# Kernel optimization log

Measured on AMD Instinct MI355X. Metric: run time of the kernel, lower is better.

Reference implementation:

```python
import jax, jax.numpy as jnp
import numpy as np

D, H, BS, K_TOP = 2560, 32, 32, 16
HD = D // H  # 80
B, S = 2, 1024
SCALE = HD ** -0.5


def setup_inputs() -> dict:
    key = jax.random.key(0)
    ks = jax.random.split(key, 10)
    sc = 0.02

    def lin(k, i, o):
        return (jax.random.normal(k, (i, o), jnp.float32) * sc,
                jnp.zeros((o,), jnp.float32))

    Wq, bq = lin(ks[0], D, D)
    Wk, bk = lin(ks[1], D, D)
    Wv, bv = lin(ks[2], D, D)
    Wo, bo = lin(ks[3], D, D)
    comp_W1, comp_b1 = lin(ks[4], BS * HD, 4 * HD)
    comp_W2, comp_b2 = lin(ks[5], 4 * HD, HD)
    comp_pos = jax.random.normal(ks[6], (BS, HD), jnp.float32) * sc
    gate_W1, gate_b1 = lin(ks[7], D, D // 2)
    gate_W2, gate_b2 = lin(ks[8], D // 2, 3)
    hidden_states = jax.random.normal(ks[9], (B, S, D), jnp.float32)
    return dict(hidden_states=hidden_states, Wq=Wq, bq=bq, Wk=Wk, bk=bk,
                Wv=Wv, bv=bv, Wo=Wo, bo=bo, comp_pos=comp_pos,
                comp_W1=comp_W1, comp_b1=comp_b1, comp_W2=comp_W2,
                comp_b2=comp_b2, gate_W1=gate_W1, gate_b1=gate_b1,
                gate_W2=gate_W2, gate_b2=gate_b2)


def reference(hidden_states, Wq, bq, Wk, bk, Wv, bv, Wo, bo, comp_pos,
              comp_W1, comp_b1, comp_W2, comp_b2, gate_W1, gate_b1,
              gate_W2, gate_b2):
    b, s, dm = hidden_states.shape
    blocks = s // BS

    def heads(y):  # [b,s,D] -> [b,H,s,hd]
        return y.reshape(b, s, H, HD).transpose(0, 2, 1, 3)

    q = heads(hidden_states @ Wq + bq)
    k = heads(hidden_states @ Wk + bk)
    v = heads(hidden_states @ Wv + bv)

    # --- compression branch: per-head block compression MLP (shared K/V) ---
    def compress(t):  # [b,H,s,hd] -> [b,H,blocks,hd]
        tb = t.reshape(b, H, blocks, BS, HD) + comp_pos  # pos emb per block slot
        tb = tb.reshape(b, H, blocks, BS * HD)
        h1 = jax.nn.gelu(tb @ comp_W1 + comp_b1, approximate=False)
        return h1 @ comp_W2 + comp_b2

    kc = compress(k)
    vc = compress(v)
    attn_c = jax.nn.softmax(jnp.einsum('bhsd,bhnd->bhsn', q, kc) * SCALE, axis=-1)
    out_c = jnp.einsum('bhsn,bhnd->bhsd', attn_c, vc)

    # --- dense scores, shared by selection scoring and window branch ---
    scores = jnp.einsum('bhqd,bhkd->bhqk', q, k) * SCALE  # [b,H,s,s]

    # --- selection branch: per-query top-k blocks by block-mean score ---
    block_scores = scores.reshape(b, H, s, blocks, BS).mean(-1)  # [b,H,s,blocks]
    _, top_idx = jax.lax.top_k(block_scores, K_TOP)  # [b,H,s,K]
    sel = (jnp.arange(blocks)[None, None, None, None, :] == top_idx[..., None]).any(-2)
    key_mask = jnp.repeat(sel, BS, axis=-1)  # [b,H,s,s]
    sel_scores = jnp.where(key_mask, scores, -jnp.inf)
    out_s = jnp.einsum('bhqk,bhkd->bhqd', jax.nn.softmax(sel_scores, axis=-1), v)

    # --- window branch: source's window mask is all-ones -> full attention ---
    out_w = jnp.einsum('bhqk,bhkd->bhqd', jax.nn.softmax(scores, axis=-1), v)

    # --- learned gates ---
    gh = jax.nn.gelu(hidden_states @ gate_W1 + gate_b1, approximate=False)
    gates = jax.nn.sigmoid(gh @ gate_W2 + gate_b2)  # [b,s,3]
    g = gates.transpose(2, 0, 1)[:, :, None, :, None]  # [3,b,1,s,1]
    combined = g[0] * out_c + g[1] * out_s + g[2] * out_w  # [b,H,s,hd]
    combined = combined.transpose(0, 2, 1, 3).reshape(b, s, dm)
    return combined @ Wo + bo
```

## Files before the change

### kernel.cpp

```cpp
#include <hip/hip_runtime.h>
#include <hip/hip_bf16.h>
#include <math.h>

typedef unsigned short u16;
typedef short v8s __attribute__((ext_vector_type(8)));
typedef float v4f __attribute__((ext_vector_type(4)));

#define SCALE_F 0.11180339887498949f

__device__ __forceinline__ float bf2f(u16 x) {
    unsigned int u = ((unsigned int)x) << 16;
    return __builtin_bit_cast(float, u);
}
__device__ __forceinline__ u16 f2bf(float f) {
    unsigned int u = __builtin_bit_cast(unsigned int, f);
    unsigned int r = (u + 0x7FFFu + ((u >> 16) & 1u)) >> 16;
    return (u16)r;
}
__device__ __forceinline__ float scrub(float v) {
    return (fabsf(v) < 1e30f) ? v : 0.f;
}
__device__ __forceinline__ v8s zero8() {
    union { v8s v; short s[8]; } t;
#pragma unroll
    for (int i = 0; i < 8; i++) t.s[i] = 0;
    return t.v;
}

__global__ void convX_kernel(const float* __restrict__ X, u16* __restrict__ Xb, int n)
{
    int i = (blockIdx.x * 256 + threadIdx.x) * 4;
    if (i >= n) return;
    float4 v = *(const float4*)(X + i);
    u16 o[4] = { f2bf(v.x), f2bf(v.y), f2bf(v.z), f2bf(v.w) };
    *(uint2*)(Xb + i) = *(uint2*)o;
}

__global__ __launch_bounds__(256) void convT_kernel(
    const float* __restrict__ W, u16* __restrict__ WT, int K, int N)
{
    __shared__ float t[32][33];
    int n0 = blockIdx.x * 32, k0 = blockIdx.y * 32;
    int tx = threadIdx.x & 31, ty = threadIdx.x >> 5;
    for (int i = ty; i < 32; i += 8) {
        int k = k0 + i, n = n0 + tx;
        t[i][tx] = (k < K && n < N) ? W[(size_t)k * N + n] : 0.f;
    }
    __syncthreads();
    for (int i = ty; i < 32; i += 8) {
        int n = n0 + i, k = k0 + tx;
        if (n < N && k < K) WT[(size_t)n * K + k] = f2bf(t[tx][i]);
    }
}

__global__ void xmean_kernel(const float* __restrict__ X, float* __restrict__ Xm)
{
    int c = blockIdx.x * 256 + threadIdx.x;
    if (c >= 2560) return;
    int g = blockIdx.y;
    const float* base = X + (size_t)g * 32 * 2560 + c;
    float s = 0.f;
#pragma unroll 4
    for (int j = 0; j < 32; j++) s += base[(size_t)j * 2560];
    Xm[(size_t)g * 2560 + c] = s * (1.f / 32.f);
}

__global__ __launch_bounds__(256) void gemmS_kernel(
    const float* __restrict__ A, const float* __restrict__ B,
    const float* __restrict__ bias, int M, int N, int K, float* __restrict__ outf)
{
    __shared__ __align__(16) u16 Ah[64][32], Al[64][32];
    __shared__ __align__(16) u16 Bh[64][32], Bl[64][32];
    const int tid = threadIdx.x;
    const int bm = blockIdx.x * 64, bn = blockIdx.y * 64;
    const int w = tid >> 6, lane = tid & 63;
    const int quad = lane >> 4, l = lane & 15;
    v4f acc[4];
#pragma unroll
    for (int nt = 0; nt < 4; nt++)
#pragma unroll
        for (int r = 0; r < 4; r++) acc[nt][r] = 0.f;
    const int ar = tid >> 2, ak = (tid & 3) * 8;
    const int kr = tid >> 3, nc = (tid & 7) * 8;
    for (int k0 = 0; k0 < K; k0 += 32) {
        float4 a0 = *(const float4*)(A + (size_t)(bm + ar) * K + (k0 + ak));
        float4 a1 = *(const float4*)(A + (size_t)(bm + ar) * K + (k0 + ak) + 4);
        float4 b0 = *(const float4*)(B + (size_t)(k0 + kr) * N + (bn + nc));
        float4 b1 = *(const float4*)(B + (size_t)(k0 + kr) * N + (bn + nc) + 4);
        float av[8] = {a0.x,a0.y,a0.z,a0.w,a1.x,a1.y,a1.z,a1.w};
        float bv[8] = {b0.x,b0.y,b0.z,b0.w,b1.x,b1.y,b1.z,b1.w};
        __syncthreads();
#pragma unroll
        for (int j = 0; j < 8; j++) {
            u16 h = f2bf(av[j]);
            Ah[ar][ak + j] = h; Al[ar][ak + j] = f2bf(av[j] - bf2f(h));
            u16 g = f2bf(bv[j]);
            Bh[nc + j][kr] = g; Bl[nc + j][kr] = f2bf(bv[j] - bf2f(g));
        }
        __syncthreads();
        v8s ah = *(const v8s*)(&Ah[w * 16 + l][quad * 8]);
        v8s al = *(const v8s*)(&Al[w * 16 + l][quad * 8]);
#pragma unroll
        for (int nt = 0; nt < 4; nt++) {
            v8s bh = *(const v8s*)(&Bh[nt * 16 + l][quad * 8]);
            v8s bl = *(const v8s*)(&Bl[nt * 16 + l][quad * 8]);
            acc[nt] = __builtin_amdgcn_mfma_f32_16x16x32_bf16(ah, bh, acc[nt], 0, 0, 0);
            acc[nt] = __builtin_amdgcn_mfma_f32_16x16x32_bf16(ah, bl, acc[nt], 0, 0, 0);
            acc[nt] = __builtin_amdgcn_mfma_f32_16x16x32_bf16(al, bh, acc[nt], 0, 0, 0);
        }
    }
#pragma unroll
    for (int nt = 0; nt < 4; nt++) {
        int col = bn + nt * 16 + l;
        float bvs = bias[col];
#pragma unroll
        for (int r = 0; r < 4; r++) {
            int row = bm + w * 16 + quad * 4 + r;
            outf[(size_t)row * N + col] = scrub(acc[nt][r] + bvs);
        }
    }
}

__global__ __launch_bounds__(256) void m1_kernel(
    const float* __restrict__ Wq, const float* __restrict__ km,
    u16* __restrict__ M1hT, u16* __restrict__ M1lT)
{
    __shared__ float Ws[64][81];
    __shared__ float Ks[32][80];
    int k0 = blockIdx.x * 64, h = blockIdx.y, b = blockIdx.z;
    int tid = threadIdx.x;
    for (int i = tid; i < 64 * 80; i += 256) {
        int kk = i / 80, dd = i - kk * 80;
        Ws[kk][dd] = Wq[(size_t)(k0 + kk) * 2560 + h * 80 + dd];
    }
    for (int i = tid; i < 32 * 80; i += 256) {
        int bl = i / 80, dd = i - bl * 80;
        Ks[bl][dd] = km[(size_t)((b << 5) + bl) * 2560 + h * 80 + dd];
    }
    __syncthreads();
    int kk = tid & 63, bq4 = tid >> 6;
    for (int bt = 0; bt < 8; bt++) {
        int blk = bt * 4 + bq4;
        float s = 0.f;
#pragma unroll 8
        for (int d = 0; d < 80; d++) s += Ws[kk][d] * Ks[blk][d];
        u16 hi = f2bf(s);
        size_t o = (size_t)(b * 1024 + h * 32 + blk) * 2560 + k0 + kk;
        M1hT[o] = hi;
        M1lT[o] = f2bf(s - bf2f(hi));
    }
}

__global__ void bias3_kernel(const float* __restrict__ bq, const float* __restrict__ km,
                             float* __restrict__ bias3)
{
    int i = blockIdx.x * 256 + threadIdx.x;
    if (i >= 2048) return;
    int b = i >> 10, hb = i & 1023, h = hb >> 5, blk = hb & 31;
    float s = 0.f;
    for (int d = 0; d < 80; d++) s += bq[h * 80 + d] * km[(size_t)((b << 5) + blk) * 2560 + h * 80 + d];
    bias3[i] = s;
}

__global__ __launch_bounds__(256) void gemmS2_kernel(
    const float* __restrict__ A, const u16* __restrict__ BhT, const u16* __restrict__ BlT,
    const float* __restrict__ bias, int M, int N, int K, float* __restrict__ outf)
{
    __shared__ __align__(16) u16 Ah[64][32], Al[64][32];
    __shared__ __align__(16) u16 Bh[64][32], Bl[64][32];
    const int tid = threadIdx.x;
    const int bm = blockIdx.x * 64, bn = blockIdx.y * 64;
    const int w = tid >> 6, lane = tid & 63;
    const int quad = lane >> 4, l = lane & 15;
    v4f acc[4];
#pragma unroll
    for (int nt = 0; nt < 4; nt++)
#pragma unroll
        for (int r = 0; r < 4; r++) acc[nt][r] = 0.f;
    const int ar = tid >> 2, ak = (tid & 3) * 8;
    for (int k0 = 0; k0 < K; k0 += 32) {
        float4 a0 = *(const float4*)(A + (size_t)(bm + ar) * K + (k0 + ak));
        float4 a1 = *(const float4*)(A + (size_t)(bm + ar) * K + (k0 + ak) + 4);
        float av[8] = {a0.x,a0.y,a0.z,a0.w,a1.x,a1.y,a1.z,a1.w};
        uint4 bh8 = *(const uint4*)(BhT + (size_t)(bn + ar) * K + (k0 + ak));
        uint4 bl8 = *(const uint4*)(BlT + (size_t)(bn + ar) * K + (k0 + ak));
        __syncthreads();
#pragma unroll
        for (int j = 0; j < 8; j++) {
            u16 h = f2bf(av[j]);
            Ah[ar][ak + j] = h; Al[ar][ak + j] = f2bf(av[j] - bf2f(h));
        }
        *(uint4*)(&Bh[ar][ak]) = bh8;
        *(uint4*)(&Bl[ar][ak]) = bl8;
        __syncthreads();
        v8s ah = *(const v8s*)(&Ah[w * 16 + l][quad * 8]);
        v8s al = *(const v8s*)(&Al[w * 16 + l][quad * 8]);
#pragma unroll
        for (int nt = 0; nt < 4; nt++) {
            v8s bh = *(const v8s*)(&Bh[nt * 16 + l][quad * 8]);
            v8s bl = *(const v8s*)(&Bl[nt * 16 + l][quad * 8]);
            acc[nt] = __builtin_amdgcn_mfma_f32_16x16x32_bf16(ah, bh, acc[nt], 0, 0, 0);
            acc[nt] = __builtin_amdgcn_mfma_f32_16x16x32_bf16(ah, bl, acc[nt], 0, 0, 0);
            acc[nt] = __builtin_amdgcn_mfma_f32_16x16x32_bf16(al, bh, acc[nt], 0, 0, 0);
        }
    }
#pragma unroll
    for (int nt = 0; nt < 4; nt++) {
        int col = bn + nt * 16 + l;
        float bvs = bias[col];
#pragma unroll
        for (int r = 0; r < 4; r++) {
            int row = bm + w * 16 + quad * 4 + r;
            outf[(size_t)row * N + col] = scrub(acc[nt][r] + bvs);
        }
    }
}

__global__ __launch_bounds__(256) void gemmB_kernel(
    const u16* __restrict__ A, const u16* __restrict__ Al2, const u16* __restrict__ BT,
    const float* __restrict__ bias, int M, int N, int K, int act, int ldc,
    u16* __restrict__ outb, float* __restrict__ outf, u16* __restrict__ outT)
{
    __shared__ __align__(16) u16 As[64][32];
    __shared__ __align__(16) u16 As2[64][32];
    __shared__ __align__(16) u16 Bs[64][32];
    const int tid = threadIdx.x;
    const int bm = blockIdx.x * 64, bn = blockIdx.y * 64;
    const int w = tid >> 6, lane = tid & 63;
    const int quad = lane >> 4, l = lane & 15;
    v4f acc[4];
#pragma unroll
    for (int nt = 0; nt < 4; nt++)
#pragma unroll
        for (int r = 0; r < 4; r++) acc[nt][r] = 0.f;
    const int ar = tid >> 2, ak = (tid & 3) * 8;
    for (int k0 = 0; k0 < K; k0 += 32) {
        uint4 av = *(const uint4*)(A + (size_t)(bm + ar) * K + (k0 + ak));
        uint4 av2 = make_uint4(0,0,0,0);
        if (Al2) av2 = *(const uint4*)(Al2 + (size_t)(bm + ar) * K + (k0 + ak));
        uint4 bv = make_uint4(0,0,0,0);
        if (bn + ar < N) bv = *(const uint4*)(BT + (size_t)(bn + ar) * K + (k0 + ak));
        __syncthreads();
        *(uint4*)(&As[ar][ak]) = av;
        if (Al2) *(uint4*)(&As2[ar][ak]) = av2;
        *(uint4*)(&Bs[ar][ak]) = bv;
        __syncthreads();
        v8s af = *(const v8s*)(&As[w * 16 + l][quad * 8]);
#pragma unroll
        for (int nt = 0; nt < 4; nt++) {
            v8s bf = *(const v8s*)(&Bs[nt * 16 + l][quad * 8]);
            acc[nt] = __builtin_amdgcn_mfma_f32_16x16x32_bf16(af, bf, acc[nt], 0, 0, 0);
        }
        if (Al2) {
            v8s af2 = *(const v8s*)(&As2[w * 16 + l][quad * 8]);
#pragma unroll
            for (int nt = 0; nt < 4; nt++) {
                v8s bf = *(const v8s*)(&Bs[nt * 16 + l][quad * 8]);
                acc[nt] = __builtin_amdgcn_mfma_f32_16x16x32_bf16(af2, bf, acc[nt], 0, 0, 0);
            }
        }
    }
#pragma unroll
    for (int nt = 0; nt < 4; nt++) {
        int col = bn + nt * 16 + l;
        if (col < N) {
            float bvs = bias[col];
#pragma unroll
            for (int r = 0; r < 4; r++) {
                int row = bm + w * 16 + quad * 4 + r;
                float c = acc[nt][r] + bvs;
                if (act == 1) c = 0.5f * c * (1.0f + erff(c * 0.70710678118654752f));
                c = scrub(c);
                if (outf) outf[(size_t)row * ldc + col] = c;
                if (outb) outb[(size_t)row * ldc + col] = f2bf(c);
                if (outT) {
                    int bb = row >> 10, s = row & 1023;
                    int hh = col / 80, dd = col - hh * 80;
                    outT[((size_t)((bb << 5) + hh) * 96 + dd) * 1024 + s] = f2bf(c);
                }
            }
        }
    }
}

__global__ void padv_kernel(u16* __restrict__ vt)
{
    int i = blockIdx.x * 256 + threadIdx.x;
    if (i >= 64 * 16 * 1024) return;
    int s = i & 1023, rr = (i >> 10) & 15, bh = i >> 14;
    vt[((size_t)bh * 96 + 80 + rr) * 1024 + s] = (rr == 0) ? (u16)0x3F80 : (u16)0;
}

__global__ void gatherF_kernel(const u16* __restrict__ src, const float* __restrict__ pos,
                               u16* __restrict__ F)
{
    int row = blockIdx.y;
    int col = blockIdx.x * 256 + threadIdx.x;
    if (col >= 2560) return;
    int b = row >> 10, h = (row >> 5) & 31, blk = row & 31;
    int j = col / 80, d = col - j * 80;
    float v = bf2f(src[(size_t)(b * 1024 + blk * 32 + j) * 2560 + h * 80 + d]) + pos[col];
    F[(size_t)row * 2560 + col] = f2bf(v);
}
__global__ void gatherFT_kernel(const u16* __restrict__ vt, const float* __restrict__ pos,
                                u16* __restrict__ F)
{
    int row = blockIdx.y;
    int col = blockIdx.x * 256 + threadIdx.x;
    if (col >= 2560) return;
    int b = row >> 10, h = (row >> 5) & 31, blk = row & 31;
    int j = col / 80, d = col - j * 80;
    float v = bf2f(vt[((size_t)((b << 5) + h) * 96 + d) * 1024 + blk * 32 + j]) + pos[col];
    F[(size_t)row * 2560 + col] = f2bf(v);
}

__global__ __launch_bounds__(256) void gates_kernel(
    const u16* __restrict__ gh, const float* __restrict__ W2,
    const float* __restrict__ b2, float* __restrict__ gates)
{
    int w = threadIdx.x >> 6, lane = threadIdx.x & 63;
    int token = blockIdx.x * 4 + w;
    float s0 = 0.f, s1 = 0.f, s2 = 0.f;
    for (int i = lane; i < 1280; i += 64) {
        float g = bf2f(gh[(size_t)token * 1280 + i]);
        s0 += g * W2[i * 3 + 0];
        s1 += g * W2[i * 3 + 1];
        s2 += g * W2[i * 3 + 2];
    }
#pragma unroll
    for (int m = 1; m < 64; m <<= 1) {
        s0 += __shfl_xor(s0, m);
        s1 += __shfl_xor(s1, m);
        s2 += __shfl_xor(s2, m);
    }
    if (lane == 0) {
        gates[token * 3 + 0] = scrub(1.f / (1.f + expf(-(s0 + b2[0]))));
        gates[token * 3 + 1] = scrub(1.f / (1.f + expf(-(s1 + b2[1]))));
        gates[token * 3 + 2] = scrub(1.f / (1.f + expf(-(s2 + b2[2]))));
    }
}

__global__ __launch_bounds__(64) void attn_kernel(
    const u16* __restrict__ qb, const u16* __restrict__ kbf,
    const u16* __restrict__ vt, const u16* __restrict__ kc,
    const u16* __restrict__ vc, const float* __restrict__ BSf,
    const float* __restrict__ gates, u16* __restrict__ comb, u16* __restrict__ combl)
{
    const int lane = threadIdx.x, quad = lane >> 4, l = lane & 15;
    const int qt = blockIdx.x, bh = blockIdx.y, b = bh >> 5, h = bh & 31;
    const float NEG = -1e30f;

    __shared__ float bs[16][33];
    __shared__ unsigned int selmask[16];
    __shared__ __align__(16) u16 Pw[16][40];

    {
        const float* bsrow = BSf + ((size_t)b * 1024 + qt * 16 + l) * 1024 + h * 32 + quad * 8;
#pragma unroll
        for (int i = 0; i < 8; i++) bs[l][quad * 8 + i] = bsrow[i] * SCALE_F;
    }
    __syncthreads();
    if (lane < 16) {
        unsigned int mask = 0u;
        for (int it = 0; it < 16; it++) {
            float best = NEG; int bi = -1;
            for (int n = 0; n < 32; n++) {
                if (((mask >> n) & 1u) == 0u && bs[lane][n] > best) { best = bs[lane][n]; bi = n; }
            }
            if (bi < 0) { for (int n = 0; n < 32; n++) if (((mask >> n) & 1u) == 0u) { bi = n; break; } }
            mask |= (1u << bi);
        }
        selmask[lane] = mask;
    }
    __syncthreads();
    const unsigned int selm_l = selmask[l];
    unsigned int selm[4];
#pragma unroll
    for (int r = 0; r < 4; r++) selm[r] = selmask[quad * 4 + r];
    (void)selm;

    v8s qfrag[3];
    {
        const u16* qrow = qb + (size_t)(b * 1024 + qt * 16 + l) * 2560 + h * 80;
#pragma unroll
        for (int c = 0; c < 3; c++) {
            if (c == 2 && quad >= 2) { qfrag[c] = zero8(); }
            else qfrag[c] = *(const v8s*)(qrow + c * 32 + quad * 8);
        }
    }

    v4f oc[5];
#pragma unroll
    for (int t = 0; t < 5; t++)
#pragma unroll
        for (int r = 0; r < 4; r++) oc[t][r] = 0.f;
    float l_c[4];
    {
        v4f s0, s1;
#pragma unroll
        for (int r = 0; r < 4; r++) { s0[r] = 0.f; s1[r] = 0.f; }
#pragma unroll
        for (int c = 0; c < 3; c++) {
            v8s b0, b1;
            if (c == 2 && quad >= 2) { b0 = zero8(); b1 = zero8(); }
            else {
                b0 = *(const v8s*)(kc + (size_t)(bh * 32 + l) * 80 + c * 32 + quad * 8);
                b1 = *(const v8s*)(kc + (size_t)(bh * 32 + 16 + l) * 80 + c * 32 + quad * 8);
            }
            s0 = __builtin_amdgcn_mfma_f32_16x16x32_bf16(qfrag[c], b0, s0, 0, 0, 0);
            s1 = __builtin_amdgcn_mfma_f32_16x16x32_bf16(qfrag[c], b1, s1, 0, 0, 0);
        }
#pragma unroll
        for (int r = 0; r < 4; r++) {
            float x0 = s0[r] * SCALE_F, x1 = s1[r] * SCALE_F;
            float mx = fmaxf(x0, x1);
#pragma unroll
            for (int m = 1; m < 16; m <<= 1) mx = fmaxf(mx, __shfl_xor(mx, m));
            float p0 = expf(x0 - mx), p1 = expf(x1 - mx);
            float sm = p0 + p1;
#pragma unroll
            for (int m = 1; m < 16; m <<= 1) sm += __shfl_xor(sm, m);
            l_c[r] = sm;
            Pw[quad * 4 + r][l]      = f2bf(p0);
            Pw[quad * 4 + r][l + 16] = f2bf(p1);
        }
        __syncthreads();
        v8s pa = *(const v8s*)(&Pw[l][quad * 8]);
#pragma unroll
        for (int t = 0; t < 5; t++) {
            union { v8s v; short s[8]; } vf;
#pragma unroll
            for (int j = 0; j < 8; j++)
                vf.s[j] = (short)vc[(size_t)(bh * 32 + quad * 8 + j) * 80 + t * 16 + l];
            oc[t] = __builtin_amdgcn_mfma_f32_16x16x32_bf16(pa, vf.v, oc[t], 0, 0, 0);
        }
        __syncthreads();
    }

    v4f aw[6], as_[6];
    float m_w[4];
#pragma unroll
    for (int r = 0; r < 4; r++) m_w[r] = NEG;
#pragma unroll
    for (int t = 0; t < 6; t++)
#pragma unroll
        for (int r = 0; r < 4; r++) { aw[t][r] = 0.f; as_[t][r] = 0.f; }

    const u16* vtp = vt + (size_t)bh * 96 * 1024;

    for (int kb = 0; kb < 32; kb++) {
        v4f s0, s1;
#pragma unroll
        for (int r = 0; r < 4; r++) { s0[r] = 0.f; s1[r] = 0.f; }
#pragma unroll
        for (int c = 0; c < 3; c++) {
            v8s k0f, k1f;
            if (c == 2 && quad >= 2) { k0f = zero8(); k1f = zero8(); }
            else {
                size_t base = (size_t)(b * 1024 + kb * 32) * 2560 + h * 80 + c * 32 + quad * 8;
                k0f = *(const v8s*)(kbf + base + (size_t)l * 2560);
                k1f = *(const v8s*)(kbf + base + (size_t)(16 + l) * 2560);
            }
            s0 = __builtin_amdgcn_mfma_f32_16x16x32_bf16(qfrag[c], k0f, s0, 0, 0, 0);
            s1 = __builtin_amdgcn_mfma_f32_16x16x32_bf16(qfrag[c], k1f, s1, 0, 0, 0);
        }
        float alw[4];
#pragma unroll
        for (int r = 0; r < 4; r++) {
            float x0 = s0[r] * SCALE_F, x1 = s1[r] * SCALE_F;
            float mb = fmaxf(x0, x1);
#pragma unroll
            for (int m = 1; m < 16; m <<= 1) mb = fmaxf(mb, __shfl_xor(mb, m));
            float mn = fmaxf(m_w[r], mb);
            alw[r] = expf(m_w[r] - mn);
            m_w[r] = mn;
            Pw[quad * 4 + r][l]      = f2bf(expf(x0 - mn));
            Pw[quad * 4 + r][l + 16] = f2bf(expf(x1 - mn));
        }
        __syncthreads();
        v8s pwa = *(const v8s*)(&Pw[l][quad * 8]);
        v8s psa = ((selm_l >> kb) & 1u) ? pwa : zero8();
#pragma unroll
        for (int t = 0; t < 6; t++) {
            v8s vfr = *(const v8s*)(vtp + ((size_t)(t * 16 + l)) * 1024 + kb * 32 + quad * 8);
#pragma unroll
            for (int r = 0; r < 4; r++) { aw[t][r] *= alw[r]; as_[t][r] *= alw[r]; }
            aw[t]  = __builtin_amdgcn_mfma_f32_16x16x32_bf16(pwa, vfr, aw[t], 0, 0, 0);
            as_[t] = __builtin_amdgcn_mfma_f32_16x16x32_bf16(psa, vfr, as_[t], 0, 0, 0);
        }
        __syncthreads();
    }

    float l_w[4], l_s[4];
#pragma unroll
    for (int r = 0; r < 4; r++) {
        l_w[r] = __shfl(aw[5][r], quad * 16);
        l_s[r] = __shfl(as_[5][r], quad * 16);
    }

#pragma unroll
    for (int r = 0; r < 4; r++) {
        int token = b * 1024 + qt * 16 + quad * 4 + r;
        float g0 = gates[token * 3 + 0], g1 = gates[token * 3 + 1], g2 = gates[token * 3 + 2];
        float inv_w = 1.f / fmaxf(l_w[r], 1e-30f);
        float inv_s = 1.f / fmaxf(l_s[r], 1e-30f);
        float inv_c = 1.f / fmaxf(l_c[r], 1e-30f);
#pragma unroll
        for (int t = 0; t < 5; t++) {
            float val = g0 * (oc[t][r] * inv_c) + g1 * (as_[t][r] * inv_s) + g2 * (aw[t][r] * inv_w);
            val = scrub(val);
            u16 hi = f2bf(val);
            size_t o = (size_t)token * 2560 + h * 80 + t * 16 + l;
            comb[o] = hi;
            combl[o] = f2bf(val - bf2f(hi));
        }
    }
}

extern "C" void kernel_launch(void* const* d_in, const int* in_sizes, int n_in,
                              void* d_out, int out_size, void* d_ws, size_t ws_size,
                              hipStream_t stream)
{
    (void)in_sizes; (void)n_in; (void)out_size; (void)ws_size;

    const float* X   = (const float*)d_in[0];
    const float* Wq  = (const float*)d_in[1];
    const float* bq  = (const float*)d_in[2];
    const float* Wk  = (const float*)d_in[3];
    const float* bk  = (const float*)d_in[4];
    const float* Wv  = (const float*)d_in[5];
    const float* bv  = (const float*)d_in[6];
    const float* Wo  = (const float*)d_in[7];
    const float* bo  = (const float*)d_in[8];
    const float* pos = (const float*)d_in[9];
    const float* cW1 = (const float*)d_in[10];
    const float* cb1 = (const float*)d_in[11];
    const float* cW2 = (const float*)d_in[12];
    const float* cb2 = (const float*)d_in[13];
    const float* gW1 = (const float*)d_in[14];
    const float* gb1 = (const float*)d_in[15];
    const float* gW2 = (const float*)d_in[16];
    const float* gb2 = (const float*)d_in[17];

    char* ws = (char*)d_ws;
    size_t off = 0;
    auto alloc = [&](size_t bytes) -> void* {
        void* p = ws + off;
        off += (bytes + 255) & ~(size_t)255;
        return p;
    };
    u16*   Xb     = (u16*)  alloc(2048ull * 2560 * 2);
    u16*   WqT    = (u16*)  alloc(2560ull * 2560 * 2);
    u16*   WkT    = (u16*)  alloc(2560ull * 2560 * 2);
    u16*   WvT    = (u16*)  alloc(2560ull * 2560 * 2);
    u16*   WoT    = (u16*)  alloc(2560ull * 2560 * 2);
    u16*   gW1T   = (u16*)  alloc(1280ull * 2560 * 2);
    u16*   cW1T   = (u16*)  alloc(320ull * 2560 * 2);
    u16*   cW2T   = (u16*)  alloc(96ull * 320 * 2);
    float* Xm     = (float*)alloc(64ull * 2560 * 4);
    float* kmeanS = (float*)alloc(64ull * 2560 * 4);
    u16*   M1hT   = (u16*)  alloc(2048ull * 2560 * 2);
    u16*   M1lT   = (u16*)  alloc(2048ull * 2560 * 2);
    float* bias3  = (float*)alloc(2048ull * 4);
    u16*   qbuf   = (u16*)  alloc(2048ull * 2560 * 2);
    u16*   kbf    = (u16*)  alloc(2048ull * 2560 * 2);
    u16*   vtb    = (u16*)  alloc(64ull * 96 * 1024 * 2);
    u16*   combl  = (u16*)  alloc(2048ull * 2560 * 2);
    char*  R1     = (char*) alloc(12ull * 1024 * 1024);
    u16*   gh     = (u16*)R1;
    u16*   Fb     = (u16*)R1;
    u16*   H1     = (u16*)(R1 + 10ull * 1024 * 1024);
    u16*   combb  = (u16*)R1;
    u16*   KC     = (u16*)  alloc(2048ull * 80 * 2);
    u16*   VC     = (u16*)  alloc(2048ull * 80 * 2);
    float* gatesf = (float*)alloc(2048ull * 3 * 4);
    float* BSf    = (float*)d_out;

    dim3 blk(256);
    convX_kernel<<<2048 * 2560 / 4 / 256, blk, 0, stream>>>(X, Xb, 2048 * 2560);
    convT_kernel<<<dim3(80, 80), blk, 0, stream>>>(Wq, WqT, 2560, 2560);
    convT_kernel<<<dim3(80, 80), blk, 0, stream>>>(Wk, WkT, 2560, 2560);
    convT_kernel<<<dim3(80, 80), blk, 0, stream>>>(Wv, WvT, 2560, 2560);
    convT_kernel<<<dim3(80, 80), blk, 0, stream>>>(Wo, WoT, 2560, 2560);
    convT_kernel<<<dim3(40, 80), blk, 0, stream>>>(gW1, gW1T, 2560, 1280);
    convT_kernel<<<dim3(10, 80), blk, 0, stream>>>(cW1, cW1T, 2560, 320);
    convT_kernel<<<dim3(3, 10), blk, 0, stream>>>(cW2, cW2T, 320, 80);
    xmean_kernel<<<dim3(10, 64), blk, 0, stream>>>(X, Xm);
    gemmS_kernel<<<dim3(1, 40), blk, 0, stream>>>(Xm, Wk, bk, 64, 2560, 2560, kmeanS);
    m1_kernel<<<dim3(40, 32, 2), blk, 0, stream>>>(Wq, kmeanS, M1hT, M1lT);
    bias3_kernel<<<8, blk, 0, stream>>>(bq, kmeanS, bias3);
    for (int b = 0; b < 2; b++) {
        gemmS2_kernel<<<dim3(16, 16), blk, 0, stream>>>(
            X + (size_t)b * 1024 * 2560, M1hT + (size_t)b * 1024 * 2560,
            M1lT + (size_t)b * 1024 * 2560, bias3 + b * 1024,
            1024, 1024, 2560, BSf + (size_t)b * 1024 * 1024);
    }
    gemmB_kernel<<<dim3(32, 40), blk, 0, stream>>>(Xb, nullptr, WqT, bq, 2048, 2560, 2560, 0, 2560, qbuf, nullptr, nullptr);
    gemmB_kernel<<<dim3(32, 40), blk, 0, stream>>>(Xb, nullptr, WkT, bk, 2048, 2560, 2560, 0, 2560, kbf, nullptr, nullptr);
    gemmB_kernel<<<dim3(32, 40), blk, 0, stream>>>(Xb, nullptr, WvT, bv, 2048, 2560, 2560, 0, 2560, nullptr, nullptr, vtb);
    padv_kernel<<<4096, blk, 0, stream>>>(vtb);
    gemmB_kernel<<<dim3(32, 20), blk, 0, stream>>>(Xb, nullptr, gW1T, gb1, 2048, 1280, 2560, 1, 1280, gh, nullptr, nullptr);
    gates_kernel<<<512, blk, 0, stream>>>(gh, gW2, gb2, gatesf);
    gatherF_kernel<<<dim3(10, 2048), blk, 0, stream>>>(kbf, pos, Fb);
    gemmB_kernel<<<dim3(32, 5), blk, 0, stream>>>(Fb, nullptr, cW1T, cb1, 2048, 320, 2560, 1, 320, H1, nullptr, nullptr);
    gemmB_kernel<<<dim3(32, 2), blk, 0, stream>>>(H1, nullptr, cW2T, cb2, 2048, 80, 320, 0, 80, KC, nullptr, nullptr);
    gatherFT_kernel<<<dim3(10, 2048), blk, 0, stream>>>(vtb, pos, Fb);
    gemmB_kernel<<<dim3(32, 5), blk, 0, stream>>>(Fb, nullptr, cW1T, cb1, 2048, 320, 2560, 1, 320, H1, nullptr, nullptr);
    gemmB_kernel<<<dim3(32, 2), blk, 0, stream>>>(H1, nullptr, cW2T, cb2, 2048, 80, 320, 0, 80, VC, nullptr, nullptr);
    attn_kernel<<<dim3(64, 64), 64, 0, stream>>>(qbuf, kbf, vtb, KC, VC, BSf, gatesf, combb, combl);
    gemmB_kernel<<<dim3(32, 40), blk, 0, stream>>>(combb, combl, WoT, bo, 2048, 2560, 2560, 0, 2560, nullptr, (float*)d_out, nullptr);
}
```

Before: 1.250 ms.

## Use direct global-to-LDS loads in GEMM and streamline attention softmax

```diff
diff --git a/kernel.cpp b/kernel.cpp
--- a/kernel.cpp
+++ b/kernel.cpp
@@ -7,6 +7,7 @@
 typedef float v4f __attribute__((ext_vector_type(4)));
 
 #define SCALE_F 0.11180339887498949f
+#define SCALE_L2 0.16129821534f
 
 __device__ __forceinline__ float bf2f(u16 x) {
     unsigned int u = ((unsigned int)x) << 16;
@@ -25,6 +26,11 @@
 #pragma unroll
     for (int i = 0; i < 8; i++) t.s[i] = 0;
     return t.v;
+}
+__device__ __forceinline__ void glds16(const void* g, void* s) {
+    __builtin_amdgcn_global_load_lds(
+        (const __attribute__((address_space(1))) unsigned int*)g,
+        (__attribute__((address_space(3))) unsigned int*)s, 16, 0, 0);
 }
 
 __global__ void convX_kernel(const float* __restrict__ X, u16* __restrict__ Xb, int n)
@@ -234,16 +240,18 @@
 #pragma unroll
         for (int r = 0; r < 4; r++) acc[nt][r] = 0.f;
     const int ar = tid >> 2, ak = (tid & 3) * 8;
+    const int brow = (bn + ar < N) ? (bn + ar) : (N - 1);
+    const u16* Ap = A + (size_t)(bm + ar) * K + ak;
+    const u16* Bp = BT + (size_t)brow * K + ak;
+    const u16* A2p = Al2 ? (Al2 + (size_t)(bm + ar) * K + ak) : nullptr;
+    char* AsW  = ((char*)As)  + w * 1024;
+    char* As2W = ((char*)As2) + w * 1024;
+    char* BsW  = ((char*)Bs)  + w * 1024;
     for (int k0 = 0; k0 < K; k0 += 32) {
-        uint4 av = *(const uint4*)(A + (size_t)(bm + ar) * K + (k0 + ak));
-        uint4 av2 = make_uint4(0,0,0,0);
-        if (Al2) av2 = *(const uint4*)(Al2 + (size_t)(bm + ar) * K + (k0 + ak));
-        uint4 bv = make_uint4(0,0,0,0);
-        if (bn + ar < N) bv = *(const uint4*)(BT + (size_t)(bn + ar) * K + (k0 + ak));
-        __syncthreads();
-        *(uint4*)(&As[ar][ak]) = av;
-        if (Al2) *(uint4*)(&As2[ar][ak]) = av2;
-        *(uint4*)(&Bs[ar][ak]) = bv;
+        __syncthreads();
+        glds16(Ap + k0, AsW);
+        glds16(Bp + k0, BsW);
+        if (Al2) glds16(A2p + k0, As2W);
         __syncthreads();
         v8s af = *(const v8s*)(&As[w * 16 + l][quad * 8]);
 #pragma unroll
@@ -283,14 +291,6 @@
     }
 }
 
-__global__ void padv_kernel(u16* __restrict__ vt)
-{
-    int i = blockIdx.x * 256 + threadIdx.x;
-    if (i >= 64 * 16 * 1024) return;
-    int s = i & 1023, rr = (i >> 10) & 15, bh = i >> 14;
-    vt[((size_t)bh * 96 + 80 + rr) * 1024 + s] = (rr == 0) ? (u16)0x3F80 : (u16)0;
-}
-
 __global__ void gatherF_kernel(const u16* __restrict__ src, const float* __restrict__ pos,
                                u16* __restrict__ F)
 {
@@ -353,6 +353,7 @@
     __shared__ float bs[16][33];
     __shared__ unsigned int selmask[16];
     __shared__ __align__(16) u16 Pw[16][40];
+    __shared__ float ocn[16][80];
 
     {
         const float* bsrow = BSf + ((size_t)b * 1024 + qt * 16 + l) * 1024 + h * 32 + quad * 8;
@@ -377,7 +378,6 @@
     unsigned int selm[4];
 #pragma unroll
     for (int r = 0; r < 4; r++) selm[r] = selmask[quad * 4 + r];
-    (void)selm;
 
     v8s qfrag[3];
     {
@@ -389,13 +389,13 @@
         }
     }
 
-    v4f oc[5];
-#pragma unroll
-    for (int t = 0; t < 5; t++)
-#pragma unroll
-        for (int r = 0; r < 4; r++) oc[t][r] = 0.f;
-    float l_c[4];
     {
+        v4f oc[5];
+#pragma unroll
+        for (int t = 0; t < 5; t++)
+#pragma unroll
+            for (int r = 0; r < 4; r++) oc[t][r] = 0.f;
+        float l_c[4];
         v4f s0, s1;
 #pragma unroll
         for (int r = 0; r < 4; r++) { s0[r] = 0.f; s1[r] = 0.f; }
@@ -412,11 +412,11 @@
         }
 #pragma unroll
         for (int r = 0; r < 4; r++) {
-            float x0 = s0[r] * SCALE_F, x1 = s1[r] * SCALE_F;
+            float x0 = s0[r] * SCALE_L2, x1 = s1[r] * SCALE_L2;
             float mx = fmaxf(x0, x1);
 #pragma unroll
             for (int m = 1; m < 16; m <<= 1) mx = fmaxf(mx, __shfl_xor(mx, m));
-            float p0 = expf(x0 - mx), p1 = expf(x1 - mx);
+            float p0 = exp2f(x0 - mx), p1 = exp2f(x1 - mx);
             float sm = p0 + p1;
 #pragma unroll
             for (int m = 1; m < 16; m <<= 1) sm += __shfl_xor(sm, m);
@@ -434,15 +434,23 @@
                 vf.s[j] = (short)vc[(size_t)(bh * 32 + quad * 8 + j) * 80 + t * 16 + l];
             oc[t] = __builtin_amdgcn_mfma_f32_16x16x32_bf16(pa, vf.v, oc[t], 0, 0, 0);
         }
-        __syncthreads();
-    }
-
-    v4f aw[6], as_[6];
-    float m_w[4];
-#pragma unroll
-    for (int r = 0; r < 4; r++) m_w[r] = NEG;
-#pragma unroll
-    for (int t = 0; t < 6; t++)
+#pragma unroll
+        for (int r = 0; r < 4; r++) {
+            int token = b * 1024 + qt * 16 + quad * 4 + r;
+            float g0 = gates[token * 3 + 0];
+            float fc = g0 / fmaxf(l_c[r], 1e-30f);
+#pragma unroll
+            for (int t = 0; t < 5; t++) ocn[quad * 4 + r][t * 16 + l] = oc[t][r] * fc;
+        }
+        __syncthreads();
+    }
+
+    v4f aw[5], as_[5];
+    float m_w[4], l_w[4], l_s[4];
+#pragma unroll
+    for (int r = 0; r < 4; r++) { m_w[r] = NEG; l_w[r] = 0.f; l_s[r] = 0.f; }
+#pragma unroll
+    for (int t = 0; t < 5; t++)
 #pragma unroll
         for (int r = 0; r < 4; r++) { aw[t][r] = 0.f; as_[t][r] = 0.f; }
 
@@ -464,50 +472,71 @@
             s0 = __builtin_amdgcn_mfma_f32_16x16x32_bf16(qfrag[c], k0f, s0, 0, 0, 0);
             s1 = __builtin_amdgcn_mfma_f32_16x16x32_bf16(qfrag[c], k1f, s1, 0, 0, 0);
         }
-        float alw[4];
+        float x0a[4], x1a[4], pmax[4];
+        float needmax = NEG;
 #pragma unroll
         for (int r = 0; r < 4; r++) {
-            float x0 = s0[r] * SCALE_F, x1 = s1[r] * SCALE_F;
-            float mb = fmaxf(x0, x1);
+            x0a[r] = s0[r] * SCALE_L2; x1a[r] = s1[r] * SCALE_L2;
+            float mb = fmaxf(x0a[r], x1a[r]);
 #pragma unroll
             for (int m = 1; m < 16; m <<= 1) mb = fmaxf(mb, __shfl_xor(mb, m));
-            float mn = fmaxf(m_w[r], mb);
-            alw[r] = expf(m_w[r] - mn);
-            m_w[r] = mn;
-            Pw[quad * 4 + r][l]      = f2bf(expf(x0 - mn));
-            Pw[quad * 4 + r][l + 16] = f2bf(expf(x1 - mn));
+            pmax[r] = mb;
+            needmax = fmaxf(needmax, mb - m_w[r]);
+        }
+        if (__all(needmax <= 8.0f)) {
+#pragma unroll
+            for (int r = 0; r < 4; r++) {
+                float p0 = exp2f(x0a[r] - m_w[r]), p1 = exp2f(x1a[r] - m_w[r]);
+                Pw[quad * 4 + r][l]      = f2bf(p0);
+                Pw[quad * 4 + r][l + 16] = f2bf(p1);
+                float st = p0 + p1;
+#pragma unroll
+                for (int m = 1; m < 16; m <<= 1) st += __shfl_xor(st, m);
+                l_w[r] += st;
+                if ((selm[r] >> kb) & 1u) l_s[r] += st;
+            }
+        } else {
+            float alw[4];
+#pragma unroll
+            for (int r = 0; r < 4; r++) {
+                float mn = fmaxf(m_w[r], pmax[r]);
+                alw[r] = exp2f(m_w[r] - mn);
+                m_w[r] = mn;
+                float p0 = exp2f(x0a[r] - mn), p1 = exp2f(x1a[r] - mn);
+                Pw[quad * 4 + r][l]      = f2bf(p0);
+                Pw[quad * 4 + r][l + 16] = f2bf(p1);
+                float st = p0 + p1;
+#pragma unroll
+                for (int m = 1; m < 16; m <<= 1) st += __shfl_xor(st, m);
+                l_w[r] = l_w[r] * alw[r] + st;
+                l_s[r] = l_s[r] * alw[r] + (((selm[r] >> kb) & 1u) ? st : 0.f);
+            }
+#pragma unroll
+            for (int t = 0; t < 5; t++)
+#pragma unroll
+                for (int r = 0; r < 4; r++) { aw[t][r] *= alw[r]; as_[t][r] *= alw[r]; }
         }
         __syncthreads();
         v8s pwa = *(const v8s*)(&Pw[l][quad * 8]);
         v8s psa = ((selm_l >> kb) & 1u) ? pwa : zero8();
 #pragma unroll
-        for (int t = 0; t < 6; t++) {
+        for (int t = 0; t < 5; t++) {
             v8s vfr = *(const v8s*)(vtp + ((size_t)(t * 16 + l)) * 1024 + kb * 32 + quad * 8);
-#pragma unroll
-            for (int r = 0; r < 4; r++) { aw[t][r] *= alw[r]; as_[t][r] *= alw[r]; }
             aw[t]  = __builtin_amdgcn_mfma_f32_16x16x32_bf16(pwa, vfr, aw[t], 0, 0, 0);
             as_[t] = __builtin_amdgcn_mfma_f32_16x16x32_bf16(psa, vfr, as_[t], 0, 0, 0);
         }
         __syncthreads();
     }
 
-    float l_w[4], l_s[4];
-#pragma unroll
-    for (int r = 0; r < 4; r++) {
-        l_w[r] = __shfl(aw[5][r], quad * 16);
-        l_s[r] = __shfl(as_[5][r], quad * 16);
-    }
-
 #pragma unroll
     for (int r = 0; r < 4; r++) {
         int token = b * 1024 + qt * 16 + quad * 4 + r;
-        float g0 = gates[token * 3 + 0], g1 = gates[token * 3 + 1], g2 = gates[token * 3 + 2];
-        float inv_w = 1.f / fmaxf(l_w[r], 1e-30f);
-        float inv_s = 1.f / fmaxf(l_s[r], 1e-30f);
-        float inv_c = 1.f / fmaxf(l_c[r], 1e-30f);
+        float g1 = gates[token * 3 + 1], g2 = gates[token * 3 + 2];
+        float fw = g2 / fmaxf(l_w[r], 1e-30f);
+        float fs = g1 / fmaxf(l_s[r], 1e-30f);
 #pragma unroll
         for (int t = 0; t < 5; t++) {
-            float val = g0 * (oc[t][r] * inv_c) + g1 * (as_[t][r] * inv_s) + g2 * (aw[t][r] * inv_w);
+            float val = ocn[quad * 4 + r][t * 16 + l] + fs * as_[t][r] + fw * aw[t][r];
             val = scrub(val);
             u16 hi = f2bf(val);
             size_t o = (size_t)token * 2560 + h * 80 + t * 16 + l;
@@ -598,7 +627,6 @@
     gemmB_kernel<<<dim3(32, 40), blk, 0, stream>>>(Xb, nullptr, WqT, bq, 2048, 2560, 2560, 0, 2560, qbuf, nullptr, nullptr);
     gemmB_kernel<<<dim3(32, 40), blk, 0, stream>>>(Xb, nullptr, WkT, bk, 2048, 2560, 2560, 0, 2560, kbf, nullptr, nullptr);
     gemmB_kernel<<<dim3(32, 40), blk, 0, stream>>>(Xb, nullptr, WvT, bv, 2048, 2560, 2560, 0, 2560, nullptr, nullptr, vtb);
-    padv_kernel<<<4096, blk, 0, stream>>>(vtb);
     gemmB_kernel<<<dim3(32, 20), blk, 0, stream>>>(Xb, nullptr, gW1T, gb1, 2048, 1280, 2560, 1, 1280, gh, nullptr, nullptr);
     gates_kernel<<<512, blk, 0, stream>>>(gh, gW2, gb2, gatesf);
     gatherF_kernel<<<dim3(10, 2048), blk, 0, stream>>>(kbf, pos, Fb);
```

Result: faster. 1.185 ms (-5.2%).
